# Kernel tuning notes

Hardware: AMD Instinct MI355X
Metric: run time of the kernel (lower is better)

## Reference

```python
import jax, jax.numpy as jnp
import numpy as np

D_MODEL = 1024
N_HEADS = 16
HEAD_DIM = D_MODEL // N_HEADS
ROPE_THETA = 10000.0


def _rope_cache(seq_len, head_dim, dtype, theta=ROPE_THETA):
    half = head_dim // 2
    inv_freq = 1.0 / theta ** (jnp.arange(half, dtype=jnp.float32) / half)
    t = jnp.arange(seq_len, dtype=jnp.float32)
    freqs = jnp.outer(t, inv_freq)                 # [L, half]
    emb = jnp.concatenate([freqs, freqs], axis=-1)  # [L, head_dim]
    return jnp.cos(emb).astype(dtype), jnp.sin(emb).astype(dtype)


def _rotate_half(x):
    d = x.shape[-1]
    x1, x2 = x[..., : d // 2], x[..., d // 2 :]
    return jnp.concatenate([-x2, x1], axis=-1)


def _apply_rope(x, cos, sin):
    return x * cos + _rotate_half(x) * sin


def setup_inputs() -> dict:
    key = jax.random.key(0)
    ks = jax.random.split(key, 9)
    B, L, D = 2, 2048, D_MODEL
    s = 1.0 / np.sqrt(D)
    return {
        "x": jax.random.normal(ks[0], (B, L, D), dtype=jnp.float32),
        "Wq": jax.random.normal(ks[1], (D, D), dtype=jnp.float32) * s,
        "bq": jnp.zeros((D,), dtype=jnp.float32),
        "Wk": jax.random.normal(ks[2], (D, D), dtype=jnp.float32) * s,
        "bk": jnp.zeros((D,), dtype=jnp.float32),
        "Wv": jax.random.normal(ks[3], (D, D), dtype=jnp.float32) * s,
        "bv": jnp.zeros((D,), dtype=jnp.float32),
        "Wo": jax.random.normal(ks[4], (D, D), dtype=jnp.float32) * s,
        "bo": jnp.zeros((D,), dtype=jnp.float32),
    }


def reference(x, Wq, bq, Wk, bk, Wv, bv, Wo, bo):
    B, L, D = x.shape
    H, Hd = N_HEADS, HEAD_DIM
    scale = Hd ** -0.5

    def proj(W, b):
        # [B,L,D] -> [B,H,L,Hd]
        return (x @ W.T + b).reshape(B, L, H, Hd).transpose(0, 2, 1, 3)

    q = proj(Wq, bq)
    k = proj(Wk, bk)
    v = proj(Wv, bv)

    cos, sin = _rope_cache(L, Hd, x.dtype)  # [L, Hd]
    q = _apply_rope(q, cos, sin)
    k = _apply_rope(k, cos, sin)

    scores = jnp.einsum("bhqd,bhkd->bhqk", q, k) * scale  # [B,H,L,L]
    attn = jax.nn.softmax(scores, axis=-1)
    ctx = jnp.einsum("bhqk,bhkd->bhqd", attn, v)           # [B,H,L,Hd]
    ctx = ctx.transpose(0, 2, 1, 3).reshape(B, L, D)
    return ctx @ Wo.T + bo
```

## Files before the change

kernel.cpp:

```cpp
#include <hip/hip_runtime.h>

typedef unsigned short u16;
typedef unsigned int u32;
typedef __attribute__((ext_vector_type(8))) __bf16 bf16v8;
typedef __attribute__((ext_vector_type(4))) __bf16 bf16v4;
typedef __attribute__((ext_vector_type(4))) float f32x4;
typedef __attribute__((ext_vector_type(16))) float f32x16;
typedef __attribute__((ext_vector_type(2))) unsigned u32x2;

#define SEQ    2048
#define NBATCH 2
#define NHEAD  16
#define HD     64
#define DM     1024
#define MROWS  4096

__device__ __forceinline__ u16 f2bf(float f) {
  unsigned int u = __float_as_uint(f);
  u += 0x7FFFu + ((u >> 16) & 1u);
  return (u16)(u >> 16);
}

__device__ __forceinline__ void gll16(const void* g, void* l) {
  __builtin_amdgcn_global_load_lds(
      (__attribute__((address_space(1))) void*)g,
      (__attribute__((address_space(3))) void*)l, 16, 0, 0);
}

__global__ __launch_bounds__(256) void k_prep(
    const float* __restrict__ x,
    const float* __restrict__ Wq, const float* __restrict__ Wk,
    const float* __restrict__ Wv, const float* __restrict__ Wo,
    u16* __restrict__ Xb, u16* __restrict__ Wqb, u16* __restrict__ Wkb,
    u16* __restrict__ Wvb, u16* __restrict__ Wob,
    float* __restrict__ cosT, float* __restrict__ sinT) {
  int bid = blockIdx.x;
  if (bid < MROWS * DM / 1024) {
    int i = bid * 256 + threadIdx.x;
    float4 v = ((const float4*)x)[i];
    ushort4 o;
    o.x = f2bf(v.x); o.y = f2bf(v.y); o.z = f2bf(v.z); o.w = f2bf(v.w);
    ((ushort4*)Xb)[i] = o;
    return;
  }
  bid -= MROWS * DM / 1024;
  if (bid < 4 * (DM * DM / 1024)) {
    int seg = bid >> 10;
    int i = (bid & 1023) * 256 + threadIdx.x;
    const float* src = (seg == 0) ? Wq : (seg == 1) ? Wk : (seg == 2) ? Wv : Wo;
    u16* dst = (seg == 0) ? Wqb : (seg == 1) ? Wkb : (seg == 2) ? Wvb : Wob;
    float4 v = ((const float4*)src)[i];
    ushort4 o;
    o.x = f2bf(v.x); o.y = f2bf(v.y); o.z = f2bf(v.z); o.w = f2bf(v.w);
    ((ushort4*)dst)[i] = o;
    return;
  }
  bid -= 4 * (DM * DM / 1024);
  int idx = bid * 256 + threadIdx.x;
  int l = idx >> 5, d = idx & 31;
  float inv = 1.0f / powf(10000.0f, (float)d * (1.0f / 32.0f));
  float ang = (float)l * inv;
  float s, c;
  sincosf(ang, &s, &c);
  cosT[idx] = c;
  sinT[idx] = s;
}

__global__ __launch_bounds__(256) void k_gemm_qkv(
    const u16* __restrict__ A,
    const u16* W0, const u16* W1, const u16* W2,
    const float* b0, const float* b1, const float* b2,
    u16* __restrict__ Qr, u16* __restrict__ Kg, u16* __restrict__ Vg,
    const float* __restrict__ cosT, const float* __restrict__ sinT) {
  __shared__ __attribute__((aligned(16))) u16 As[128 * 64];
  __shared__ __attribute__((aligned(16))) u16 Bs[128 * 64];
  const int z = blockIdx.z;
  const u16* W = (z == 0) ? W0 : ((z == 1) ? W1 : W2);
  const float* bias = (z == 0) ? b0 : ((z == 1) ? b1 : b2);

  const int tid = threadIdx.x;
  const int lane = tid & 63, wid = tid >> 6;
  const int g = lane >> 4, c = lane & 15;
  const int wm = wid >> 1, wn = wid & 1;
  const int bm = blockIdx.x, bn = blockIdx.y;

  const f32x4 vz = {0.f, 0.f, 0.f, 0.f};
  f32x4 acc[4][4];
#pragma unroll
  for (int i = 0; i < 4; i++)
#pragma unroll
    for (int j = 0; j < 4; j++) acc[i][j] = vz;

  const int srow = tid >> 3;
  const int scb = tid & 7;

  for (int kt = 0; kt < DM / 64; ++kt) {
    __syncthreads();
#pragma unroll
    for (int cc = 0; cc < 4; ++cc) {
      int row = cc * 32 + srow;
      int sc = scb ^ (row & 7);
      gll16(A + (size_t)(bm * 128 + row) * DM + kt * 64 + sc * 8,
            &As[cc * 2048 + wid * 512]);
      gll16(W + (size_t)(bn * 128 + row) * DM + kt * 64 + sc * 8,
            &Bs[cc * 2048 + wid * 512]);
    }
    __syncthreads();
#pragma unroll
    for (int kk = 0; kk < 2; ++kk) {
      bf16v8 av[4], bv[4];
#pragma unroll
      for (int i = 0; i < 4; i++) {
        int row = wm * 64 + i * 16 + c;
        int sc = (kk * 4 + g) ^ (row & 7);
        av[i] = *(const bf16v8*)&As[row * 64 + sc * 8];
      }
#pragma unroll
      for (int j = 0; j < 4; j++) {
        int row = wn * 64 + j * 16 + c;
        int sc = (kk * 4 + g) ^ (row & 7);
        bv[j] = *(const bf16v8*)&Bs[row * 64 + sc * 8];
      }
#pragma unroll
      for (int i = 0; i < 4; i++)
#pragma unroll
        for (int j = 0; j < 4; j++)
          acc[i][j] = __builtin_amdgcn_mfma_f32_16x16x32_bf16(av[i], bv[j], acc[i][j], 0, 0, 0);
    }
  }

  if (z == 2) {
    const int h = bn * 2 + wn;
#pragma unroll
    for (int i = 0; i < 4; i++) {
      int m0 = bm * 128 + wm * 64 + i * 16 + g * 4;
#pragma unroll
      for (int r = 0; r < 4; r++) {
        int m = m0 + r;
        int tok = m & (SEQ - 1);
        int b = m >> 11;
        size_t base = ((size_t)((b * NHEAD + h) * 256 + (tok >> 3)) * 64) * 8 + (tok & 7);
#pragma unroll
        for (int j = 0; j < 4; j++) {
          int d = j * 16 + c;
          Vg[base + (size_t)d * 8] = f2bf(acc[i][j][r] + bias[bn * 128 + wn * 64 + d]);
        }
      }
    }
  } else if (z == 1) {
    const int h = bn * 2 + wn;
    const int nb = bn * 128 + wn * 64;
#pragma unroll
    for (int i = 0; i < 4; i++) {
      int m0 = bm * 128 + wm * 64 + i * 16 + g * 4;
#pragma unroll
      for (int r = 0; r < 4; r++) {
        int m = m0 + r;
        int tok = m & (SEQ - 1);
        int b = m >> 11;
        size_t bhb = (size_t)(b * NHEAD + h) * 8;
#pragma unroll
        for (int j = 0; j < 2; j++) {
          int d = j * 16 + c;
          float x1 = acc[i][j][r] + bias[nb + d];
          float x2 = acc[i][j + 2][r] + bias[nb + d + 32];
          float cs = cosT[tok * 32 + d];
          float sn = sinT[tok * 32 + d];
          Kg[(bhb + (d >> 3)) * (SEQ * 8) + tok * 8 + (d & 7)]     = f2bf(x1 * cs - x2 * sn);
          Kg[(bhb + 4 + (d >> 3)) * (SEQ * 8) + tok * 8 + (d & 7)] = f2bf(x2 * cs + x1 * sn);
        }
      }
    }
  } else {
    const float qs = 0.180336880f;
    const int h = bn * 2 + wn;
    const int nb = bn * 128 + wn * 64;
#pragma unroll
    for (int i = 0; i < 4; i++) {
      int m0 = bm * 128 + wm * 64 + i * 16 + g * 4;
#pragma unroll
      for (int r = 0; r < 4; r++) {
        int m = m0 + r;
        int tok = m & (SEQ - 1);
        int b = m >> 11;
        size_t obase = ((size_t)(b * NHEAD + h) * SEQ + tok) * HD;
#pragma unroll
        for (int j = 0; j < 2; j++) {
          int d = j * 16 + c;
          float x1 = acc[i][j][r] + bias[nb + d];
          float x2 = acc[i][j + 2][r] + bias[nb + d + 32];
          float cs = cosT[tok * 32 + d];
          float sn = sinT[tok * 32 + d];
          Qr[obase + d]      = f2bf((x1 * cs - x2 * sn) * qs);
          Qr[obase + d + 32] = f2bf((x2 * cs + x1 * sn) * qs);
        }
      }
    }
  }
}

__global__ __launch_bounds__(256) void k_gemm_out(
    const u16* __restrict__ A, const u16* __restrict__ W,
    const float* __restrict__ bias, float* __restrict__ out) {
  __shared__ __attribute__((aligned(16))) u16 As[128 * 64];
  __shared__ __attribute__((aligned(16))) u16 Bs[128 * 64];
  const int tid = threadIdx.x;
  const int lane = tid & 63, wid = tid >> 6;
  const int g = lane >> 4, c = lane & 15;
  const int wm = wid >> 1, wn = wid & 1;
  const int bm = blockIdx.x, bn = blockIdx.y;

  const f32x4 vz = {0.f, 0.f, 0.f, 0.f};
  f32x4 acc[4][4];
#pragma unroll
  for (int i = 0; i < 4; i++)
#pragma unroll
    for (int j = 0; j < 4; j++) acc[i][j] = vz;

  const int srow = tid >> 3;
  const int scb = tid & 7;

  for (int kt = 0; kt < DM / 64; ++kt) {
    __syncthreads();
#pragma unroll
    for (int cc = 0; cc < 4; ++cc) {
      int row = cc * 32 + srow;
      int sc = scb ^ (row & 7);
      gll16(A + (size_t)(bm * 128 + row) * DM + kt * 64 + sc * 8,
            &As[cc * 2048 + wid * 512]);
      gll16(W + (size_t)(bn * 128 + row) * DM + kt * 64 + sc * 8,
            &Bs[cc * 2048 + wid * 512]);
    }
    __syncthreads();
#pragma unroll
    for (int kk = 0; kk < 2; ++kk) {
      bf16v8 av[4], bv[4];
#pragma unroll
      for (int i = 0; i < 4; i++) {
        int row = wm * 64 + i * 16 + c;
        int sc = (kk * 4 + g) ^ (row & 7);
        av[i] = *(const bf16v8*)&As[row * 64 + sc * 8];
      }
#pragma unroll
      for (int j = 0; j < 4; j++) {
        int row = wn * 64 + j * 16 + c;
        int sc = (kk * 4 + g) ^ (row & 7);
        bv[j] = *(const bf16v8*)&Bs[row * 64 + sc * 8];
      }
#pragma unroll
      for (int i = 0; i < 4; i++)
#pragma unroll
        for (int j = 0; j < 4; j++)
          acc[i][j] = __builtin_amdgcn_mfma_f32_16x16x32_bf16(av[i], bv[j], acc[i][j], 0, 0, 0);
    }
  }

#pragma unroll
  for (int i = 0; i < 4; i++) {
    int m = bm * 128 + wm * 64 + i * 16 + g * 4;
#pragma unroll
    for (int j = 0; j < 4; j++) {
      int n = bn * 128 + wn * 64 + j * 16 + c;
      float bb = bias[n];
#pragma unroll
      for (int r = 0; r < 4; r++)
        out[(size_t)(m + r) * DM + n] = acc[i][j][r] + bb;
    }
  }
}

__global__ __launch_bounds__(512, 4) void k_attn(
    const u16* __restrict__ Qb, const u16* __restrict__ Kg,
    const u16* __restrict__ Vg, u16* __restrict__ Cb) {
  __shared__ __attribute__((aligned(16))) u16 SMEM[32768];
  const int tid = threadIdx.x, lane = tid & 63, wid = tid >> 6;
  const int hh = lane >> 5, ln = lane & 31;
  const int team = wid >> 2, lw = wid & 3;
  const int bh = blockIdx.y;
  const int q0 = blockIdx.x * 128 + lw * 32;

  const u16* Qh = Qb + ((size_t)bh * SEQ + q0 + ln) * HD + hh * 8;
  bf16v8 qf[4];
#pragma unroll
  for (int ks = 0; ks < 4; ks++) qf[ks] = *(const bf16v8*)(Qh + ks * 16);

  f32x16 octx[2];
#pragma unroll
  for (int dsub = 0; dsub < 2; dsub++)
#pragma unroll
    for (int r = 0; r < 16; r++) octx[dsub][r] = 0.f;
  f32x4 lac4 = {0.f, 0.f, 0.f, 0.f};

  const int kvbase = team * 1024;

#define STAGE(buf, kv0)                                                              \
  {                                                                                  \
    u16* Kb_ = &SMEM[(team * 2 + (buf)) * 8192];                                     \
    u16* Vb_ = Kb_ + 4096;                                                           \
    _Pragma("unroll") for (int cc = 0; cc < 2; ++cc) {                               \
      int kk = lw * 2 + cc;                                                          \
      gll16(Kg + ((size_t)(bh * 8 + kk) * SEQ + (kv0)) * 8 + lane * 8,               \
            &Kb_[kk * 512]);                                                         \
      gll16(Vg + ((size_t)(bh * 256 + ((kv0) >> 3) + kk) * 64 + lane) * 8,           \
            &Vb_[kk * 512]);                                                         \
    }                                                                                \
  }

  STAGE(0, kvbase);
  __syncthreads();
  int cur = 0;

  for (int it = 0; it < 16; ++it) {
    if (it + 1 < 16) STAGE(cur ^ 1, kvbase + (it + 1) * 64);
    const u16* Kc = &SMEM[(team * 2 + cur) * 8192];
    const u16* Vc = Kc + 4096;

    bf16v8 pb[4];
#pragma unroll
    for (int s = 0; s < 2; s++) {
      f32x16 sT;
#pragma unroll
      for (int r = 0; r < 16; r++) sT[r] = 0.f;
#pragma unroll
      for (int ks = 0; ks < 4; ks++) {
        bf16v8 kf = *(const bf16v8*)&Kc[(ks * 2 + hh) * 512 + (s * 32 + ln) * 8];
        sT = __builtin_amdgcn_mfma_f32_32x32x16_bf16(kf, qf[ks], sT, 0, 0, 0);
      }
      float p[16];
#pragma unroll
      for (int r = 0; r < 16; r++) {
        p[r] = __builtin_amdgcn_exp2f(sT[r]);
        lac4[r & 3] += p[r];
      }
#pragma unroll
      for (int ksl = 0; ksl < 2; ksl++) {
        const int bb = ksl * 8;
        u32 Aw, Bw, Cw, Dw;
        asm("v_cvt_pk_bf16_f32 %0, %1, %2" : "=v"(Aw) : "v"(p[bb + 0]), "v"(p[bb + 1]));
        asm("v_cvt_pk_bf16_f32 %0, %1, %2" : "=v"(Bw) : "v"(p[bb + 2]), "v"(p[bb + 3]));
        asm("v_cvt_pk_bf16_f32 %0, %1, %2" : "=v"(Cw) : "v"(p[bb + 4]), "v"(p[bb + 5]));
        asm("v_cvt_pk_bf16_f32 %0, %1, %2" : "=v"(Dw) : "v"(p[bb + 6]), "v"(p[bb + 7]));
        u32x2 r02 = __builtin_amdgcn_permlane32_swap(Aw, Cw, false, false);
        u32x2 r13 = __builtin_amdgcn_permlane32_swap(Bw, Dw, false, false);
        union { u32 w[4]; bf16v8 v; } pu;
        pu.w[0] = r02[0]; pu.w[1] = r13[0]; pu.w[2] = r02[1]; pu.w[3] = r13[1];
        pb[s * 2 + ksl] = pu.v;
      }
    }

#pragma unroll
    for (int dsub = 0; dsub < 2; dsub++)
#pragma unroll
      for (int ks = 0; ks < 4; ks++) {
        bf16v8 vf = *(const bf16v8*)&Vc[(ks * 2 + hh) * 512 + (dsub * 32 + ln) * 8];
        octx[dsub] = __builtin_amdgcn_mfma_f32_32x32x16_bf16(vf, pb[ks], octx[dsub], 0, 0, 0);
      }

    __syncthreads();
    cur ^= 1;
  }

  float lacc = (lac4[0] + lac4[1]) + (lac4[2] + lac4[3]);
  float lt_own = lacc + __shfl_xor(lacc, 32);

  float* Mo = (float*)SMEM;
  float* Ml = ((float*)SMEM) + 8192;
  __syncthreads();
  if (team == 1) {
#pragma unroll
    for (int dsub = 0; dsub < 2; dsub++)
#pragma unroll
      for (int rr = 0; rr < 4; rr++) {
        f32x4 v = {octx[dsub][rr * 4 + 0], octx[dsub][rr * 4 + 1],
                   octx[dsub][rr * 4 + 2], octx[dsub][rr * 4 + 3]};
        *(f32x4*)&Mo[(((lw * 8) + dsub * 4 + rr) * 64 + lane) * 4] = v;
      }
    if (hh == 0) Ml[lw * 32 + ln] = lt_own;
  }
  __syncthreads();
  if (team == 0) {
    float lt = lt_own + Ml[lw * 32 + ln];
    float inv = 1.0f / lt;
    const int b = bh >> 4, h = bh & 15;
    const int q = q0 + ln;
    u16* orow = Cb + ((size_t)(b * SEQ + q)) * DM + h * HD;
#pragma unroll
    for (int dsub = 0; dsub < 2; dsub++)
#pragma unroll
      for (int rr = 0; rr < 4; rr++) {
        f32x4 m = *(const f32x4*)&Mo[(((lw * 8) + dsub * 4 + rr) * 64 + lane) * 4];
        int d0 = dsub * 32 + rr * 8 + hh * 4;
        bf16v4 o4 = {(__bf16)((octx[dsub][rr * 4 + 0] + m[0]) * inv),
                     (__bf16)((octx[dsub][rr * 4 + 1] + m[1]) * inv),
                     (__bf16)((octx[dsub][rr * 4 + 2] + m[2]) * inv),
                     (__bf16)((octx[dsub][rr * 4 + 3] + m[3]) * inv)};
        *(bf16v4*)(orow + d0) = o4;
      }
  }
}

extern "C" void kernel_launch(void* const* d_in, const int* in_sizes, int n_in,
                              void* d_out, int out_size, void* d_ws, size_t ws_size,
                              hipStream_t stream) {
  (void)in_sizes; (void)n_in; (void)out_size;
  const float* x  = (const float*)d_in[0];
  const float* Wq = (const float*)d_in[1];
  const float* bq = (const float*)d_in[2];
  const float* Wk = (const float*)d_in[3];
  const float* bk = (const float*)d_in[4];
  const float* Wv = (const float*)d_in[5];
  const float* bv = (const float*)d_in[6];
  const float* Wo = (const float*)d_in[7];
  const float* bo = (const float*)d_in[8];
  float* out = (float*)d_out;
  char* ws = (char*)d_ws;
  const size_t MB = 1024ull * 1024ull;

  if (ws_size < 49ull * MB) return;

  float* cosT = (float*)(ws);
  float* sinT = (float*)(ws + 256 * 1024);
  u16* Xb  = (u16*)(ws + 512 * 1024);
  u16* Wqb = (u16*)(ws + 512 * 1024 + 8 * MB);
  u16* Wkb = (u16*)(ws + 512 * 1024 + 10 * MB);
  u16* Wvb = (u16*)(ws + 512 * 1024 + 12 * MB);
  u16* Wob = (u16*)(ws + 512 * 1024 + 14 * MB);
  u16* Qr  = (u16*)(ws + 512 * 1024 + 24 * MB);
  u16* Kg  = (u16*)(ws + 512 * 1024 + 32 * MB);
  u16* Vg  = (u16*)(ws + 512 * 1024 + 40 * MB);
  u16* Cb  = Xb;

  k_prep<<<dim3(8448), 256, 0, stream>>>(x, Wq, Wk, Wv, Wo, Xb, Wqb, Wkb, Wvb, Wob,
                                         cosT, sinT);

  dim3 gp(MROWS / 128, DM / 128, 3);
  k_gemm_qkv<<<gp, 256, 0, stream>>>(Xb, Wqb, Wkb, Wvb, bq, bk, bv, Qr, Kg, Vg,
                                     cosT, sinT);

  dim3 ga(SEQ / 128, NBATCH * NHEAD);
  k_attn<<<ga, 512, 0, stream>>>(Qr, Kg, Vg, Cb);

  dim3 go(MROWS / 128, DM / 128);
  k_gemm_out<<<go, 256, 0, stream>>>(Cb, Wob, bo, out);
}
```

Measured before the change: 117.9 us.

## Read K/V directly from global in attention and halve out-GEMM N tile

The attention kernel drops its double-buffered LDS staging of K and V and the per-iteration barriers. MFMA operands are now loaded straight from global memory, relying on the cache since the four waves of a team share the same K/V. Shared memory shrinks to just the cross-team reduction buffers, which may raise occupancy. The output projection GEMM moves from 128x128 to 128x64 tiles, doubling the grid to 512 blocks for better CU fill at the cost of more A re-reads and less reuse per block.

```diff
diff --git a/kernel.cpp b/kernel.cpp
--- a/kernel.cpp
+++ b/kernel.cpp
@@ -203,7 +203,7 @@
     const u16* __restrict__ A, const u16* __restrict__ W,
     const float* __restrict__ bias, float* __restrict__ out) {
   __shared__ __attribute__((aligned(16))) u16 As[128 * 64];
-  __shared__ __attribute__((aligned(16))) u16 Bs[128 * 64];
+  __shared__ __attribute__((aligned(16))) u16 Bs[64 * 64];
   const int tid = threadIdx.x;
   const int lane = tid & 63, wid = tid >> 6;
   const int g = lane >> 4, c = lane & 15;
@@ -211,11 +211,11 @@
   const int bm = blockIdx.x, bn = blockIdx.y;
 
   const f32x4 vz = {0.f, 0.f, 0.f, 0.f};
-  f32x4 acc[4][4];
+  f32x4 acc[4][2];
 #pragma unroll
   for (int i = 0; i < 4; i++)
 #pragma unroll
-    for (int j = 0; j < 4; j++) acc[i][j] = vz;
+    for (int j = 0; j < 2; j++) acc[i][j] = vz;
 
   const int srow = tid >> 3;
   const int scb = tid & 7;
@@ -228,13 +228,18 @@
       int sc = scb ^ (row & 7);
       gll16(A + (size_t)(bm * 128 + row) * DM + kt * 64 + sc * 8,
             &As[cc * 2048 + wid * 512]);
-      gll16(W + (size_t)(bn * 128 + row) * DM + kt * 64 + sc * 8,
+    }
+#pragma unroll
+    for (int cc = 0; cc < 2; ++cc) {
+      int row = cc * 32 + srow;
+      int sc = scb ^ (row & 7);
+      gll16(W + (size_t)(bn * 64 + row) * DM + kt * 64 + sc * 8,
             &Bs[cc * 2048 + wid * 512]);
     }
     __syncthreads();
 #pragma unroll
     for (int kk = 0; kk < 2; ++kk) {
-      bf16v8 av[4], bv[4];
+      bf16v8 av[4], bv[2];
 #pragma unroll
       for (int i = 0; i < 4; i++) {
         int row = wm * 64 + i * 16 + c;
@@ -242,15 +247,15 @@
         av[i] = *(const bf16v8*)&As[row * 64 + sc * 8];
       }
 #pragma unroll
-      for (int j = 0; j < 4; j++) {
-        int row = wn * 64 + j * 16 + c;
+      for (int j = 0; j < 2; j++) {
+        int row = wn * 32 + j * 16 + c;
         int sc = (kk * 4 + g) ^ (row & 7);
         bv[j] = *(const bf16v8*)&Bs[row * 64 + sc * 8];
       }
 #pragma unroll
       for (int i = 0; i < 4; i++)
 #pragma unroll
-        for (int j = 0; j < 4; j++)
+        for (int j = 0; j < 2; j++)
           acc[i][j] = __builtin_amdgcn_mfma_f32_16x16x32_bf16(av[i], bv[j], acc[i][j], 0, 0, 0);
     }
   }
@@ -259,8 +264,8 @@
   for (int i = 0; i < 4; i++) {
     int m = bm * 128 + wm * 64 + i * 16 + g * 4;
 #pragma unroll
-    for (int j = 0; j < 4; j++) {
-      int n = bn * 128 + wn * 64 + j * 16 + c;
+    for (int j = 0; j < 2; j++) {
+      int n = bn * 64 + wn * 32 + j * 16 + c;
       float bb = bias[n];
 #pragma unroll
       for (int r = 0; r < 4; r++)
@@ -272,13 +277,17 @@
 __global__ __launch_bounds__(512, 4) void k_attn(
     const u16* __restrict__ Qb, const u16* __restrict__ Kg,
     const u16* __restrict__ Vg, u16* __restrict__ Cb) {
-  __shared__ __attribute__((aligned(16))) u16 SMEM[32768];
+  __shared__ float Mo[8192];
+  __shared__ float Ml[128];
   const int tid = threadIdx.x, lane = tid & 63, wid = tid >> 6;
   const int hh = lane >> 5, ln = lane & 31;
   const int team = wid >> 2, lw = wid & 3;
   const int bh = blockIdx.y;
   const int q0 = blockIdx.x * 128 + lw * 32;
 
+  const u16* Kh = Kg + (size_t)bh * 8 * SEQ * 8;
+  const u16* Vh = Vg + (size_t)bh * 256 * 64 * 8;
+
   const u16* Qh = Qb + ((size_t)bh * SEQ + q0 + ln) * HD + hh * 8;
   bf16v8 qf[4];
 #pragma unroll
@@ -293,27 +302,8 @@
 
   const int kvbase = team * 1024;
 
-#define STAGE(buf, kv0)                                                              \
-  {                                                                                  \
-    u16* Kb_ = &SMEM[(team * 2 + (buf)) * 8192];                                     \
-    u16* Vb_ = Kb_ + 4096;                                                           \
-    _Pragma("unroll") for (int cc = 0; cc < 2; ++cc) {                               \
-      int kk = lw * 2 + cc;                                                          \
-      gll16(Kg + ((size_t)(bh * 8 + kk) * SEQ + (kv0)) * 8 + lane * 8,               \
-            &Kb_[kk * 512]);                                                         \
-      gll16(Vg + ((size_t)(bh * 256 + ((kv0) >> 3) + kk) * 64 + lane) * 8,           \
-            &Vb_[kk * 512]);                                                         \
-    }                                                                                \
-  }
-
-  STAGE(0, kvbase);
-  __syncthreads();
-  int cur = 0;
-
   for (int it = 0; it < 16; ++it) {
-    if (it + 1 < 16) STAGE(cur ^ 1, kvbase + (it + 1) * 64);
-    const u16* Kc = &SMEM[(team * 2 + cur) * 8192];
-    const u16* Vc = Kc + 4096;
+    const int kv0 = kvbase + it * 64;
 
     bf16v8 pb[4];
 #pragma unroll
@@ -323,7 +313,8 @@
       for (int r = 0; r < 16; r++) sT[r] = 0.f;
 #pragma unroll
       for (int ks = 0; ks < 4; ks++) {
-        bf16v8 kf = *(const bf16v8*)&Kc[(ks * 2 + hh) * 512 + (s * 32 + ln) * 8];
+        bf16v8 kf = *(const bf16v8*)(Kh +
+            ((size_t)(ks * 2 + hh) * SEQ + kv0 + s * 32 + ln) * 8);
         sT = __builtin_amdgcn_mfma_f32_32x32x16_bf16(kf, qf[ks], sT, 0, 0, 0);
       }
       float p[16];
@@ -352,20 +343,15 @@
     for (int dsub = 0; dsub < 2; dsub++)
 #pragma unroll
       for (int ks = 0; ks < 4; ks++) {
-        bf16v8 vf = *(const bf16v8*)&Vc[(ks * 2 + hh) * 512 + (dsub * 32 + ln) * 8];
+        bf16v8 vf = *(const bf16v8*)(Vh +
+            ((size_t)((kv0 >> 3) + ks * 2 + hh) * 64 + dsub * 32 + ln) * 8);
         octx[dsub] = __builtin_amdgcn_mfma_f32_32x32x16_bf16(vf, pb[ks], octx[dsub], 0, 0, 0);
       }
-
-    __syncthreads();
-    cur ^= 1;
   }
 
   float lacc = (lac4[0] + lac4[1]) + (lac4[2] + lac4[3]);
   float lt_own = lacc + __shfl_xor(lacc, 32);
 
-  float* Mo = (float*)SMEM;
-  float* Ml = ((float*)SMEM) + 8192;
-  __syncthreads();
   if (team == 1) {
 #pragma unroll
     for (int dsub = 0; dsub < 2; dsub++)
@@ -440,6 +426,6 @@
   dim3 ga(SEQ / 128, NBATCH * NHEAD);
   k_attn<<<ga, 512, 0, stream>>>(Qr, Kg, Vg, Cb);
 
-  dim3 go(MROWS / 128, DM / 128);
+  dim3 go(MROWS / 128, DM / 64);
   k_gemm_out<<<go, 256, 0, stream>>>(Cb, Wob, bo, out);
 }
```

Measured after the change: 145.4 us. +23.4%, slower.
